# Kernel optimization log

Measured on AMD Instinct MI355X. Metric: run time of the kernel, lower is better.

The kernel has to match this reference:

```python
import jax, jax.numpy as jnp
import numpy as np

SEQ, D_IN, D_OUT = 8192, 768, 128


def setup_inputs() -> dict:
    key = jax.random.key(0)
    k1, k2, k3, k4 = jax.random.split(key, 4)
    x = jax.random.normal(k1, (SEQ, D_IN), dtype=jnp.float32)
    # torch nn.Linear weights are stored as [d_out, d_in]
    scale = 1.0 / np.sqrt(D_IN)
    w_query = jax.random.normal(k2, (D_OUT, D_IN), dtype=jnp.float32) * scale
    w_key = jax.random.normal(k3, (D_OUT, D_IN), dtype=jnp.float32) * scale
    w_value = jax.random.normal(k4, (D_OUT, D_IN), dtype=jnp.float32) * scale
    return {"x": x, "w_query": w_query, "w_key": w_key, "w_value": w_value}


def reference(x, w_query, w_key, w_value):
    # Linear with bias=False: y = x @ W.T   (W is [d_out, d_in])
    q = x @ w_query.T                      # [N, d_out]
    k = x @ w_key.T                        # [N, d_out]
    v = x @ w_value.T                      # [N, d_out]
    inv_sqrt_d = 1.0 / jnp.sqrt(jnp.float32(k.shape[-1]))
    scores = (q @ k.T) * inv_sqrt_d        # [N, N] -- fully materialized, as in source
    weights = jax.nn.softmax(scores, axis=-1)
    return weights @ v                     # [N, d_out]
```

## Files before the change

kernel.cpp:

```cpp
#include <hip/hip_runtime.h>
#include <stdint.h>

#define SEQ 8192
#define DIN 768
#define DOUT 128

typedef __attribute__((ext_vector_type(8))) short short8;
typedef __attribute__((ext_vector_type(8))) unsigned short ushort8v;
typedef __attribute__((ext_vector_type(4))) float f32x4;

#define CEXPF (1.4426950408889634f * 0.08838834764831845f)

#if __has_builtin(__builtin_amdgcn_exp2f)
#define EXP2(x) __builtin_amdgcn_exp2f(x)
#else
#define EXP2(x) __builtin_exp2f(x)
#endif

__device__ __forceinline__ unsigned short f2bf(float f) {
  return (unsigned short)((__float_as_uint(f) + 0x8000u) >> 16);
}

__device__ __forceinline__ void gload_lds16(const void* g, void* l) {
  __builtin_amdgcn_global_load_lds(
      (const __attribute__((address_space(1))) void*)g,
      (__attribute__((address_space(3))) void*)l, 16, 0, 0);
}

__global__ void conv_kernel(const float* __restrict__ x,
                            const float* __restrict__ wq,
                            const float* __restrict__ wk,
                            const float* __restrict__ wv,
                            unsigned short* __restrict__ xb,
                            unsigned short* __restrict__ Wb) {
  int b = blockIdx.x;
  if (b < 6144) {
    int idx4 = (b * 256 + threadIdx.x) * 4;
    float4 v = *(const float4*)(x + idx4);
    ushort4 o;
    o.x = f2bf(v.x); o.y = f2bf(v.y); o.z = f2bf(v.z); o.w = f2bf(v.w);
    *(ushort4*)(xb + idx4) = o;
  } else {
    int idx4 = ((b - 6144) * 256 + threadIdx.x) * 4;
    int z = idx4 / (DOUT * DIN);
    int rem = idx4 - z * (DOUT * DIN);
    const float* src = (z == 0) ? wq : (z == 1) ? wk : wv;
    float4 v = *(const float4*)(src + rem);
    float sc = (z == 0) ? CEXPF : 1.0f;
    ushort4 o;
    o.x = f2bf(v.x * sc); o.y = f2bf(v.y * sc);
    o.z = f2bf(v.z * sc); o.w = f2bf(v.w * sc);
    *(ushort4*)(Wb + idx4) = o;
  }
}

__launch_bounds__(256, 2)
__global__ void qkv_kernel(const unsigned short* __restrict__ xb,
                           const unsigned short* __restrict__ Wb,
                           unsigned short* __restrict__ Qb,
                           unsigned short* __restrict__ Kb,
                           unsigned short* __restrict__ Vtb) {
  __shared__ unsigned char lds[65536];

  const int t    = threadIdx.x;
  const int wave = t >> 6;
  const int lane = t & 63;
  const int g    = lane >> 4;
  const int r    = lane & 15;
  const int z    = blockIdx.y;
  const int m0   = blockIdx.x * 128;
  const unsigned short* Wz = Wb + (size_t)z * DOUT * DIN;

  auto stage = [&](int buf, int kb) {
    unsigned char* xs = lds + buf * 32768;
    unsigned char* ws = xs + 16384;
#pragma unroll
    for (int c = 0; c < 4; c++) {
      int ci  = (wave * 4 + c) * 64 + lane;
      int row = ci >> 3, ch = ci & 7;
      int sc  = (ch ^ (row & 7)) << 3;
      gload_lds16(xb + (size_t)(m0 + row) * DIN + kb + sc,
                  xs + ((wave * 4 + c) << 10) + (lane << 4));
      gload_lds16(Wz + (size_t)row * DIN + kb + sc,
                  ws + ((wave * 4 + c) << 10) + (lane << 4));
    }
  };

  f32x4 acc[8][2];
#pragma unroll
  for (int mt = 0; mt < 8; mt++)
#pragma unroll
    for (int nt = 0; nt < 2; nt++) acc[mt][nt] = 0.f;

  stage(0, 0);
  asm volatile("s_waitcnt vmcnt(0)" ::: "memory");
  __builtin_amdgcn_s_barrier();
  asm volatile("" ::: "memory");

#pragma unroll 1
  for (int s = 0; s < 12; s++) {
    const int cur = s & 1;
    if (s < 11) stage(cur ^ 1, (s + 1) * 64);
    unsigned char* xs = lds + cur * 32768;
    unsigned char* ws = xs + 16384;
    __builtin_amdgcn_s_setprio(1);
#pragma unroll
    for (int kc = 0; kc < 2; kc++) {
      short8 bfr[2];
#pragma unroll
      for (int nt = 0; nt < 2; nt++) {
        int row = wave * 32 + nt * 16 + r;
        bfr[nt] = *(const short8*)(xs + row * 128 + (((kc * 4 + g) ^ (row & 7)) << 4));
      }
#pragma unroll
      for (int mt = 0; mt < 8; mt++) {
        int oc = mt * 16 + r;
        short8 afr = *(const short8*)(ws + oc * 128 + (((kc * 4 + g) ^ (oc & 7)) << 4));
        acc[mt][0] = __builtin_amdgcn_mfma_f32_16x16x32_bf16(afr, bfr[0], acc[mt][0], 0, 0, 0);
        acc[mt][1] = __builtin_amdgcn_mfma_f32_16x16x32_bf16(afr, bfr[1], acc[mt][1], 0, 0, 0);
      }
    }
    __builtin_amdgcn_s_setprio(0);
    asm volatile("s_waitcnt vmcnt(0)" ::: "memory");
    __builtin_amdgcn_s_barrier();
    asm volatile("" ::: "memory");
  }

  if (z < 2) {
    unsigned short* out = (z == 0) ? Qb : Kb;
#pragma unroll
    for (int mt = 0; mt < 8; mt++)
#pragma unroll
      for (int nt = 0; nt < 2; nt++) {
        ushort4 o;
        o.x = f2bf(acc[mt][nt][0]); o.y = f2bf(acc[mt][nt][1]);
        o.z = f2bf(acc[mt][nt][2]); o.w = f2bf(acc[mt][nt][3]);
        *(ushort4*)(out + (size_t)(m0 + wave * 32 + nt * 16 + r) * DOUT + mt * 16 + g * 4) = o;
      }
  } else {
    unsigned short* ct = (unsigned short*)(lds + wave * 8704);
#pragma unroll
    for (int mt = 0; mt < 8; mt++)
#pragma unroll
      for (int nt = 0; nt < 2; nt++) {
        ushort4 o;
        o.x = f2bf(acc[mt][nt][0]); o.y = f2bf(acc[mt][nt][1]);
        o.z = f2bf(acc[mt][nt][2]); o.w = f2bf(acc[mt][nt][3]);
        *(ushort4*)&ct[(nt * 16 + r) * 136 + mt * 16 + g * 4] = o;
      }
    __syncthreads();
#pragma unroll
    for (int pass = 0; pass < 8; pass++) {
      int col = pass * 16 + (lane >> 2);
      int ch  = lane & 3;
      ushort8v a;
#pragma unroll
      for (int i = 0; i < 8; i++) a[i] = ct[(ch * 8 + i) * 136 + col];
      *(ushort8v*)(Vtb + (size_t)col * SEQ + m0 + wave * 32 + ch * 8) = a;
    }
  }
}

__launch_bounds__(512, 4)
__global__ void attn_kernel(const unsigned short* __restrict__ Qb,
                            const unsigned short* __restrict__ Kb,
                            const unsigned short* __restrict__ Vtb,
                            float* __restrict__ Opart,
                            float* __restrict__ lpart) {
  __shared__ unsigned char lds[43008];

  const int t    = threadIdx.x;
  const int wave = t >> 6;
  const int lane = t & 63;
  const int g    = lane >> 4;
  const int r    = lane & 15;
  unsigned short* Pl = (unsigned short*)(lds + 32768 + wave * 1280);

  const int qb = blockIdx.x;
  const int sp = blockIdx.y;
  const int q0 = qb * 128 + wave * 16;
  const int kvbase = sp * 1024;

  auto stageK = [&](int buf, int kv0) {
    unsigned char* KL = lds + buf * 8192;
    int idx = (wave << 6) + lane;
    int krow = idx >> 4, kch = idx & 15;
    gload_lds16(Kb + ((size_t)(kv0 + krow) << 7) + ((kch ^ (krow & 15)) << 3),
                KL + (idx << 4));
  };
  auto stageV = [&](int buf, int kv0) {
    unsigned char* VL = lds + 16384 + buf * 8192;
    int idx = (wave << 6) + lane;
    int d = idx >> 2, c2 = idx & 3;
    int sd = (d & 3) ^ ((d >> 2) & 3);
    gload_lds16(Vtb + (size_t)d * SEQ + kv0 + ((c2 ^ sd) << 3),
                VL + (idx << 4));
  };

  short8 qf[4];
#pragma unroll
  for (int kc = 0; kc < 4; kc++)
    qf[kc] = *(const short8*)(Qb + (size_t)(q0 + r) * DOUT + kc * 32 + g * 8);

  short8 onesf;
#pragma unroll
  for (int j = 0; j < 8; j++) onesf[j] = (r == 0) ? (short)0x3F80 : (short)0;

  f32x4 oacc[8];
  f32x4 lacc = 0.f;
#pragma unroll
  for (int n = 0; n < 8; n++) oacc[n] = 0.f;

  const int sdr = (r & 3) ^ ((r >> 2) & 3);

  stageK(0, kvbase);
  stageV(0, kvbase);
  asm volatile("s_waitcnt vmcnt(0)" ::: "memory");
  __builtin_amdgcn_s_barrier();
  asm volatile("" ::: "memory");

#pragma unroll 1
  for (int it = 0; it < 32; it++) {
    const int cur = it & 1;
    if (it < 31) {
      stageK(cur ^ 1, kvbase + (it + 1) * 32);
      stageV(cur ^ 1, kvbase + (it + 1) * 32);
    }
    unsigned char* KL = lds + cur * 8192;
    unsigned char* VL = lds + 16384 + cur * 8192;

    f32x4 sf[2];
    sf[0] = 0.f; sf[1] = 0.f;
    __builtin_amdgcn_s_setprio(1);
#pragma unroll
    for (int mt = 0; mt < 2; mt++) {
      int row = mt * 16 + r;
#pragma unroll
      for (int kc = 0; kc < 4; kc++) {
        short8 kf = *(const short8*)(KL + row * 256 + (((kc * 4 + g) ^ r) << 4));
        sf[mt] = __builtin_amdgcn_mfma_f32_16x16x32_bf16(kf, qf[kc], sf[mt], 0, 0, 0);
      }
    }
    __builtin_amdgcn_s_setprio(0);

#pragma unroll
    for (int mt = 0; mt < 2; mt++) {
      ushort4 p;
      p.x = f2bf(EXP2(sf[mt][0]));
      p.y = f2bf(EXP2(sf[mt][1]));
      p.z = f2bf(EXP2(sf[mt][2]));
      p.w = f2bf(EXP2(sf[mt][3]));
      *(ushort4*)(Pl + r * 40 + mt * 16 + g * 4) = p;
    }
    short8 pf = *(const short8*)(Pl + r * 40 + g * 8);

    __builtin_amdgcn_s_setprio(1);
#pragma unroll
    for (int nt = 0; nt < 8; nt++) {
      int d = nt * 16 + r;
      short8 vf = *(const short8*)(VL + d * 64 + ((g ^ sdr) << 4));
      oacc[nt] = __builtin_amdgcn_mfma_f32_16x16x32_bf16(pf, vf, oacc[nt], 0, 0, 0);
    }
    lacc = __builtin_amdgcn_mfma_f32_16x16x32_bf16(pf, onesf, lacc, 0, 0, 0);
    __builtin_amdgcn_s_setprio(0);

    asm volatile("s_waitcnt vmcnt(0)" ::: "memory");
    __builtin_amdgcn_s_barrier();
    asm volatile("" ::: "memory");
  }

  const size_t pbase = (size_t)sp * SEQ;
#pragma unroll
  for (int rr = 0; rr < 4; rr++) {
    int qrow = q0 + g * 4 + rr;
#pragma unroll
    for (int nt = 0; nt < 8; nt++)
      Opart[(pbase + qrow) * DOUT + nt * 16 + r] = oacc[nt][rr];
    if (r == 0) lpart[pbase + qrow] = lacc[rr];
  }
}

__global__ void combine_kernel(const float* __restrict__ Opart,
                               const float* __restrict__ lpart,
                               float* __restrict__ out) {
  int idx = blockIdx.x * 256 + threadIdx.x;
  int s   = idx >> 5;
  int d4  = (idx & 31) * 4;
  float L = 0.f;
  f32x4 acc = 0.f;
#pragma unroll
  for (int p = 0; p < 8; p++) {
    L += lpart[p * SEQ + s];
    acc += *(const f32x4*)(Opart + ((size_t)p * SEQ + s) * DOUT + d4);
  }
  f32x4 res = acc * (1.0f / L);
  *(f32x4*)(out + (size_t)s * DOUT + d4) = res;
}

extern "C" void kernel_launch(void* const* d_in, const int* in_sizes, int n_in,
                              void* d_out, int out_size, void* d_ws, size_t ws_size,
                              hipStream_t stream) {
  const float* x  = (const float*)d_in[0];
  const float* wq = (const float*)d_in[1];
  const float* wk = (const float*)d_in[2];
  const float* wv = (const float*)d_in[3];
  float* out = (float*)d_out;

  unsigned short* Qb  = (unsigned short*)d_ws;
  unsigned short* Kb  = Qb + (size_t)SEQ * DOUT;
  unsigned short* Vtb = Kb + (size_t)SEQ * DOUT;
  float* Opart = (float*)(Vtb + (size_t)SEQ * DOUT);
  float* lpart = Opart + (size_t)8 * SEQ * DOUT;
  unsigned short* Wb  = (unsigned short*)Opart;
  unsigned short* xb  = Wb + (size_t)3 * DOUT * DIN;
  if (ws_size < (size_t)(6291456 + 33554432 + 262144)) return;

  conv_kernel<<<dim3(6432), 256, 0, stream>>>(x, wq, wk, wv, xb, Wb);
  qkv_kernel<<<dim3(64, 3), 256, 0, stream>>>(xb, Wb, Qb, Kb, Vtb);
  attn_kernel<<<dim3(64, 8), 512, 0, stream>>>(Qb, Kb, Vtb, Opart, lpart);
  combine_kernel<<<dim3(1024), 256, 0, stream>>>(Opart, lpart, out);
}
```

Baseline: 138.7 us.

## Double KV tile to 64 rows and single-buffer V with split barrier schedule

The attention loop now processes 64 keys per iteration instead of 32, halving the iteration count and the barriers per key. K stays double-buffered, but V moves to a single buffer that is loaded after a second barrier, so its load overlaps the next iteration's QK and softmax work. LDS use grows to about 66 KB per block, which may lower occupancy against the 4-blocks launch bound. V's load latency is now exposed only up to the next iteration's mid-loop wait.

Measured after the change: 134.0 us. -3.4%, faster.

```diff
diff --git a/kernel.cpp b/kernel.cpp
--- a/kernel.cpp
+++ b/kernel.cpp
@@ -167,14 +167,15 @@
                             const unsigned short* __restrict__ Vtb,
                             float* __restrict__ Opart,
                             float* __restrict__ lpart) {
-  __shared__ unsigned char lds[43008];
+  __shared__ unsigned char lds[67584];
 
   const int t    = threadIdx.x;
   const int wave = t >> 6;
   const int lane = t & 63;
   const int g    = lane >> 4;
   const int r    = lane & 15;
-  unsigned short* Pl = (unsigned short*)(lds + 32768 + wave * 1280);
+  unsigned short* Pl = (unsigned short*)(lds + 49152 + wave * 2304);
+  unsigned char* Vl = lds + 32768;
 
   const int qb = blockIdx.x;
   const int sp = blockIdx.y;
@@ -182,19 +183,23 @@
   const int kvbase = sp * 1024;
 
   auto stageK = [&](int buf, int kv0) {
-    unsigned char* KL = lds + buf * 8192;
-    int idx = (wave << 6) + lane;
-    int krow = idx >> 4, kch = idx & 15;
-    gload_lds16(Kb + ((size_t)(kv0 + krow) << 7) + ((kch ^ (krow & 15)) << 3),
-                KL + (idx << 4));
+    unsigned char* Kl = lds + buf * 16384;
+#pragma unroll
+    for (int c = 0; c < 2; c++) {
+      int idx = (wave * 2 + c) * 64 + lane;
+      int krow = idx >> 4, kch = idx & 15;
+      gload_lds16(Kb + ((size_t)(kv0 + krow) << 7) + ((kch ^ (krow & 15)) << 3),
+                  Kl + ((wave * 2 + c) << 10) + (lane << 4));
+    }
   };
-  auto stageV = [&](int buf, int kv0) {
-    unsigned char* VL = lds + 16384 + buf * 8192;
-    int idx = (wave << 6) + lane;
-    int d = idx >> 2, c2 = idx & 3;
-    int sd = (d & 3) ^ ((d >> 2) & 3);
-    gload_lds16(Vtb + (size_t)d * SEQ + kv0 + ((c2 ^ sd) << 3),
-                VL + (idx << 4));
+  auto stageV = [&](int kv0) {
+#pragma unroll
+    for (int c = 0; c < 2; c++) {
+      int idx = (wave * 2 + c) * 64 + lane;
+      int d = idx >> 3, c2 = idx & 7;
+      gload_lds16(Vtb + (size_t)d * SEQ + kv0 + ((c2 ^ (d & 7)) << 3),
+                  Vl + ((wave * 2 + c) << 10) + (lane << 4));
+    }
   };
 
   short8 qf[4];
@@ -211,62 +216,68 @@
 #pragma unroll
   for (int n = 0; n < 8; n++) oacc[n] = 0.f;
 
-  const int sdr = (r & 3) ^ ((r >> 2) & 3);
-
   stageK(0, kvbase);
-  stageV(0, kvbase);
+  stageV(kvbase);
   asm volatile("s_waitcnt vmcnt(0)" ::: "memory");
   __builtin_amdgcn_s_barrier();
   asm volatile("" ::: "memory");
 
 #pragma unroll 1
-  for (int it = 0; it < 32; it++) {
+  for (int it = 0; it < 16; it++) {
     const int cur = it & 1;
-    if (it < 31) {
-      stageK(cur ^ 1, kvbase + (it + 1) * 32);
-      stageV(cur ^ 1, kvbase + (it + 1) * 32);
-    }
-    unsigned char* KL = lds + cur * 8192;
-    unsigned char* VL = lds + 16384 + cur * 8192;
-
-    f32x4 sf[2];
-    sf[0] = 0.f; sf[1] = 0.f;
+    if (it < 15) stageK(cur ^ 1, kvbase + (it + 1) * 64);
+    unsigned char* Kl = lds + cur * 16384;
+
+    f32x4 sf[4];
+    sf[0] = 0.f; sf[1] = 0.f; sf[2] = 0.f; sf[3] = 0.f;
     __builtin_amdgcn_s_setprio(1);
 #pragma unroll
-    for (int mt = 0; mt < 2; mt++) {
+    for (int mt = 0; mt < 4; mt++) {
       int row = mt * 16 + r;
 #pragma unroll
       for (int kc = 0; kc < 4; kc++) {
-        short8 kf = *(const short8*)(KL + row * 256 + (((kc * 4 + g) ^ r) << 4));
+        short8 kf = *(const short8*)(Kl + row * 256 + (((kc * 4 + g) ^ (row & 15)) << 4));
         sf[mt] = __builtin_amdgcn_mfma_f32_16x16x32_bf16(kf, qf[kc], sf[mt], 0, 0, 0);
       }
     }
     __builtin_amdgcn_s_setprio(0);
 
 #pragma unroll
-    for (int mt = 0; mt < 2; mt++) {
+    for (int mt = 0; mt < 4; mt++) {
       ushort4 p;
       p.x = f2bf(EXP2(sf[mt][0]));
       p.y = f2bf(EXP2(sf[mt][1]));
       p.z = f2bf(EXP2(sf[mt][2]));
       p.w = f2bf(EXP2(sf[mt][3]));
-      *(ushort4*)(Pl + r * 40 + mt * 16 + g * 4) = p;
-    }
-    short8 pf = *(const short8*)(Pl + r * 40 + g * 8);
-
-    __builtin_amdgcn_s_setprio(1);
-#pragma unroll
-    for (int nt = 0; nt < 8; nt++) {
-      int d = nt * 16 + r;
-      short8 vf = *(const short8*)(VL + d * 64 + ((g ^ sdr) << 4));
-      oacc[nt] = __builtin_amdgcn_mfma_f32_16x16x32_bf16(pf, vf, oacc[nt], 0, 0, 0);
-    }
-    lacc = __builtin_amdgcn_mfma_f32_16x16x32_bf16(pf, onesf, lacc, 0, 0, 0);
-    __builtin_amdgcn_s_setprio(0);
+      *(ushort4*)(Pl + r * 72 + mt * 16 + g * 4) = p;
+    }
+    short8 pf[2];
+#pragma unroll
+    for (int c2 = 0; c2 < 2; c2++)
+      pf[c2] = *(const short8*)(Pl + r * 72 + c2 * 32 + g * 8);
 
     asm volatile("s_waitcnt vmcnt(0)" ::: "memory");
     __builtin_amdgcn_s_barrier();
     asm volatile("" ::: "memory");
+
+    __builtin_amdgcn_s_setprio(1);
+#pragma unroll
+    for (int nt = 0; nt < 8; nt++) {
+      int d = nt * 16 + r;
+#pragma unroll
+      for (int c2 = 0; c2 < 2; c2++) {
+        short8 vf = *(const short8*)(Vl + d * 128 + (((c2 * 4 + g) ^ (d & 7)) << 4));
+        oacc[nt] = __builtin_amdgcn_mfma_f32_16x16x32_bf16(pf[c2], vf, oacc[nt], 0, 0, 0);
+      }
+    }
+    lacc = __builtin_amdgcn_mfma_f32_16x16x32_bf16(pf[0], onesf, lacc, 0, 0, 0);
+    lacc = __builtin_amdgcn_mfma_f32_16x16x32_bf16(pf[1], onesf, lacc, 0, 0, 0);
+    __builtin_amdgcn_s_setprio(0);
+
+    asm volatile("" ::: "memory");
+    __builtin_amdgcn_s_barrier();
+    asm volatile("" ::: "memory");
+    if (it < 15) stageV(kvbase + (it + 1) * 64);
   }
 
   const size_t pbase = (size_t)sp * SEQ;
```
